# Kernel tuning notes

Measured on AMD Instinct MI355X. Metric: run time of the kernel, lower is better.

Reference implementation:

```python
import jax, jax.numpy as jnp
import numpy as np

VOCAB = 50000; T = 4096; EMBED = 500; H = 500  # hidden per direction (HIDDEN_SIZE=1000, bidirectional)
NUM_TAGS = 16; START = 14; STOP = 15
NEG = -10000.0


def setup_inputs() -> dict:
    key = jax.random.key(0)
    ks = jax.random.split(key, 16)
    n = lambda k, s, sc=0.1: (jax.random.normal(k, s) * sc).astype(jnp.float32)
    trans = n(ks[12], (NUM_TAGS, NUM_TAGS), 1.0)
    trans = trans.at[START, :].set(NEG).at[:, STOP].set(NEG)  # as in __init__
    return {
        "sent": jax.random.randint(ks[0], (T,), 0, VOCAB),
        "embed_w": n(ks[1], (VOCAB, EMBED), 1.0),
        "wih0": n(ks[2], (2, 4 * H, EMBED)),
        "whh0": n(ks[3], (2, 4 * H, H)),
        "bih0": n(ks[4], (2, 4 * H)),
        "bhh0": n(ks[5], (2, 4 * H)),
        "wih1": n(ks[6], (2, 4 * H, 2 * H)),
        "whh1": n(ks[7], (2, 4 * H, H)),
        "bih1": n(ks[8], (2, 4 * H)),
        "bhh1": n(ks[9], (2, 4 * H)),
        "w_out": n(ks[10], (NUM_TAGS, 2 * H)),
        "b_out": n(ks[11], (NUM_TAGS,)),
        "trans": trans,
        "h0": n(ks[13], (4, H), 1.0),  # init_hidden() uses randn; layout [layer*2+dir, H]
        "c0": n(ks[14], (4, H), 1.0),
    }


def _lstm_dir(x, wih, whh, bih, bhh, h0, c0):
    b = bih + bhh
    def cell(carry, xt):
        h, c = carry
        g = xt @ wih.T + h @ whh.T + b          # [4H], torch gate order i,f,g,o
        i, f, gg, o = jnp.split(g, 4)
        c = jax.nn.sigmoid(f) * c + jax.nn.sigmoid(i) * jnp.tanh(gg)
        h = jax.nn.sigmoid(o) * jnp.tanh(c)
        return (h, c), h
    _, hs = jax.lax.scan(cell, (h0, c0), x)
    return hs  # [T, H]


def _bilstm_layer(x, wih, whh, bih, bhh, h0, c0):
    fwd = _lstm_dir(x, wih[0], whh[0], bih[0], bhh[0], h0[0], c0[0])
    bwd = _lstm_dir(x[::-1], wih[1], whh[1], bih[1], bhh[1], h0[1], c0[1])[::-1]
    return jnp.concatenate([fwd, bwd], axis=-1)  # [T, 2H]


def _features(sent, embed_w, wih0, whh0, bih0, bhh0, wih1, whh1, bih1, bhh1, w_out, b_out, h0, c0):
    x = embed_w[sent]                                            # [T, EMBED]
    x = _bilstm_layer(x, wih0, whh0, bih0, bhh0, h0[0:2], c0[0:2])
    x = _bilstm_layer(x, wih1, whh1, bih1, bhh1, h0[2:4], c0[2:4])
    return x @ w_out.T + b_out                                   # [T, NUM_TAGS]


def _viterbi(feats, trans):
    score0 = jnp.full((NUM_TAGS,), NEG, dtype=feats.dtype).at[START].set(0.0)
    def step(score, feat):
        m = score[None, :] + trans               # m[tag, prev] = score[prev] + trans[tag, prev]
        return jnp.max(m, axis=1) + feat, jnp.argmax(m, axis=1)
    score, bptr = jax.lax.scan(step, score0, feats)              # bptr: [T, NUM_TAGS]
    score = score + trans[STOP]
    best_tag = jnp.argmax(score)
    best_score = score[best_tag]
    # faithful to the source backtrace: best_tag is NOT updated inside its loop,
    # so path = [bptr[1][bt], ..., bptr[T-1][bt], bt]
    path = jnp.concatenate([bptr[1:, best_tag], best_tag[None]])
    return best_score, path


def reference(sent, embed_w, wih0, whh0, bih0, bhh0, wih1, whh1, bih1, bhh1, w_out, b_out, trans, h0, c0):
    feats = _features(sent, embed_w, wih0, whh0, bih0, bhh0,
                      wih1, whh1, bih1, bhh1, w_out, b_out, h0, c0)
    return _viterbi(feats, trans)
```

## Files before the change

kernel.cpp:

```cpp
#include <hip/hip_runtime.h>


#define T_SEQ 4096
#define HPAD  512
#define NTAG  16


__global__ void zero_k(float* __restrict__ p, int n) {
  int i = blockIdx.x * blockDim.x + threadIdx.x;
  int stride = gridDim.x * blockDim.x;
  for (; i < n; i += stride) p[i] = 0.0f;
}

__global__ void embed_k(const int* __restrict__ sent, const float* __restrict__ ew,
                        float* __restrict__ x0) {
  int t = blockIdx.x;
  int row = sent[t];
  for (int k = threadIdx.x; k < HPAD; k += blockDim.x)
    x0[(size_t)t * HPAD + k] = (k < 500) ? ew[(size_t)row * 500 + k] : 0.0f;
}

__global__ __launch_bounds__(256) void gin_gemm_k(
    const float* __restrict__ A, int KA,
    const float* __restrict__ wih, const float* __restrict__ bih,
    const float* __restrict__ bhh, int Kreal, float* __restrict__ G) {
  const int dir = blockIdx.z;
  const int bm = blockIdx.y, bn = blockIdx.x;
  const float* W = wih + (size_t)dir * 2000 * Kreal;

  __shared__ float As[16][128];
  __shared__ float Bs[16][128];

  const int tid = threadIdx.x;
  const int tx = tid & 15, ty = tid >> 4;
  float acc[8][8] = {};

  for (int k0 = 0; k0 < KA; k0 += 16) {
#pragma unroll
    for (int q = 0; q < 2; q++) {
      int f4 = tid + q * 256;
      int m = f4 >> 2, kc = (f4 & 3) * 4;
      float4 av = *reinterpret_cast<const float4*>(A + (size_t)(bm * 128 + m) * KA + k0 + kc);
      As[kc + 0][m] = av.x; As[kc + 1][m] = av.y;
      As[kc + 2][m] = av.z; As[kc + 3][m] = av.w;
    }
#pragma unroll
    for (int q = 0; q < 2; q++) {
      int f4 = tid + q * 256;
      int n = f4 >> 2, kc = (f4 & 3) * 4;
      int nn = bn * 128 + n;
      int gate = nn >> 9, j = nn & 511;
#pragma unroll
      for (int e = 0; e < 4; e++) {
        int k = k0 + kc + e;
        int jk = k & 511, half = k >> 9;
        float v = 0.0f;
        if (j < 500 && jk < 500)
          v = W[(size_t)(gate * 500 + j) * Kreal + half * 500 + jk];
        Bs[kc + e][n] = v;
      }
    }
    __syncthreads();
#pragma unroll
    for (int kk = 0; kk < 16; kk++) {
      float a[8], b[8];
      *reinterpret_cast<float4*>(&a[0]) = *reinterpret_cast<const float4*>(&As[kk][ty * 8]);
      *reinterpret_cast<float4*>(&a[4]) = *reinterpret_cast<const float4*>(&As[kk][ty * 8 + 4]);
      *reinterpret_cast<float4*>(&b[0]) = *reinterpret_cast<const float4*>(&Bs[kk][tx * 8]);
      *reinterpret_cast<float4*>(&b[4]) = *reinterpret_cast<const float4*>(&Bs[kk][tx * 8 + 4]);
#pragma unroll
      for (int i = 0; i < 8; i++)
#pragma unroll
        for (int j = 0; j < 8; j++) acc[i][j] = fmaf(a[i], b[j], acc[i][j]);
    }
    __syncthreads();
  }
#pragma unroll
  for (int i = 0; i < 8; i++) {
#pragma unroll
    for (int j = 0; j < 8; j++) {
      int m = bm * 128 + ty * 8 + i;
      int nn = bn * 128 + tx * 8 + j;
      int gate = nn >> 9, ju = nn & 511;
      float o = 0.0f;
      if (ju < 500) {
        int r = gate * 500 + ju;
        o = acc[i][j] + bih[dir * 2000 + r] + bhh[dir * 2000 + r];
      }
      G[((size_t)dir * T_SEQ + m) * 2048 + nn] = o;
    }
  }
}

__device__ __forceinline__ unsigned long long pack_hv(unsigned tag, float h) {
  return (unsigned long long)tag | ((unsigned long long)__float_as_uint(h) << 32);
}

__device__ __forceinline__ float fsig(float x) {
  float e = __expf(-x);
  return __builtin_amdgcn_rcpf(1.0f + e);
}
__device__ __forceinline__ float ftanhf(float x) {
  return fmaf(2.0f, fsig(x + x), -1.0f);
}

__global__ void hinit_k(const float* __restrict__ h0, int layer,
                        unsigned long long* __restrict__ hcomm) {
  int i = blockIdx.x * blockDim.x + threadIdx.x;
  int dir = i >> 10, par = (i >> 9) & 1, j = i & 511;
  unsigned long long v;
  if (par == 0) {
    float h = (j < 500) ? h0[(layer * 2 + dir) * 500 + j] : 0.0f;
    v = pack_hv(0u, h);
  } else {
    v = 0xFFFFFFFFull;
  }
  hcomm[(size_t)(dir * 2 + par) * HPAD + j] = v;
}

__global__ __launch_bounds__(1024)
__attribute__((amdgpu_waves_per_eu(4, 4)))
void lstm_k(
    const float* __restrict__ whh_base,
    const float* __restrict__ gin,
    const float* __restrict__ c0,
    float* __restrict__ xout,
    unsigned long long* __restrict__ hcomm,
    int layer) {
  __shared__ float part[16][68];
  __shared__ float hbuf[16][32];

  const int tid = threadIdx.x;
  const int dir = blockIdx.x >> 5;
  const int wgd = blockIdx.x & 31;
  const int w = tid >> 6;
  const int lane = tid & 63;

  const int gate = lane >> 4;
  const int ul   = lane & 15;
  const int j    = wgd * 16 + ul;
  const int row  = gate * 500 + j;

  float wreg[32];
  const float* Wd = whh_base + (size_t)dir * 2000 * 500;
#pragma unroll
  for (int i = 0; i < 32; i++) {
    int k = w * 32 + i;
    wreg[i] = (j < 500 && k < 500) ? Wd[(size_t)row * 500 + k] : 0.0f;
  }
#pragma unroll
  for (int i = 0; i < 32; i++) asm volatile("" : "+v"(wreg[i]));

  float c = 0.0f;
  if (w == 0 && lane < 16 && j < 500) c = c0[(layer * 2 + dir) * 500 + j];

  unsigned long long* hcd = hcomm + (size_t)dir * 2 * HPAD;
  bool dead = false;

  for (int t = 0; t < T_SEQ; t++) {
    const int t_in = (dir == 0) ? t : (T_SEQ - 1 - t);

    float gi = 0.0f;
    if (w == 0) {
      const float* gb = gin + ((size_t)dir * T_SEQ + t_in) * 2048;
      gi = gb[gate * 512 + j];
    }

    unsigned long long v = 0;
    if (!dead) {
      const unsigned long long* hp =
          hcd + (size_t)(t & 1) * HPAD + w * 32 + (lane & 31);
      int guard = 0;
      for (;;) {
        v = __hip_atomic_load(hp, __ATOMIC_RELAXED, __HIP_MEMORY_SCOPE_AGENT);
        if (__all((int)((unsigned)v == (unsigned)t))) break;
        if (++guard > (1 << 22)) { dead = true; break; }
      }
    }
    float hval = __uint_as_float((unsigned)(v >> 32));

    if (lane < 32) hbuf[w][lane] = hval;
    float a = 0.0f;
#pragma unroll
    for (int b = 0; b < 8; b++) {
      float4 hv = *reinterpret_cast<const float4*>(&hbuf[w][b * 4]);
      a = fmaf(wreg[b * 4 + 0], hv.x, a);
      a = fmaf(wreg[b * 4 + 1], hv.y, a);
      a = fmaf(wreg[b * 4 + 2], hv.z, a);
      a = fmaf(wreg[b * 4 + 3], hv.w, a);
    }
    part[w][lane] = a;
    __syncthreads();

    if (w == 0) {
      __builtin_amdgcn_s_setprio(1);
      float s = gi;
#pragma unroll
      for (int q = 0; q < 16; q++) s += part[q][lane];
      float nl = (gate == 2) ? ftanhf(s) : fsig(s);
      float xf = __shfl(nl, lane + 16, 64);
      float xg = __shfl(nl, lane + 32, 64);
      float xo = __shfl(nl, lane + 48, 64);
      if (lane < 16) {
        c = xf * c + nl * xg;
        float h = xo * ftanhf(c);
        __hip_atomic_store(hcd + (size_t)((t + 1) & 1) * HPAD + j,
                           pack_hv((unsigned)(t + 1), h),
                           __ATOMIC_RELAXED, __HIP_MEMORY_SCOPE_AGENT);
        if (j < 500)
          xout[(size_t)t_in * 1024 + (size_t)dir * HPAD + j] = h;
      }
      __builtin_amdgcn_s_setprio(0);
    }
  }
}

__global__ __launch_bounds__(256) void feats_k(
    const float* __restrict__ x2, const float* __restrict__ w_out,
    const float* __restrict__ b_out, float* __restrict__ feats) {
  int tid = threadIdx.x;
  int tag = tid & 15, tl = tid >> 4;
  int t = blockIdx.x * 16 + tl;
  float acc = 0.0f;
  for (int k = 0; k < 1024; k++) {
    int jk = k & 511;
    if (jk < 500)
      acc = fmaf(x2[(size_t)t * 1024 + k], w_out[tag * 1000 + (k >> 9) * 500 + jk], acc);
  }
  feats[t * 16 + tag] = acc + b_out[tag];
}

__global__ __launch_bounds__(256) void viterbi_k(
    const float* __restrict__ feats, const float* __restrict__ trans,
    int* __restrict__ bptr, float* __restrict__ out) {
  __shared__ float sfin[NTAG];
  __shared__ int sbest;
  int tid = threadIdx.x;
  if (tid < 64) {
    int tag = tid & 15;
    float treg[16];
#pragma unroll
    for (int p = 0; p < 16; p++) treg[p] = trans[tag * 16 + p];
    float s = (tag == 14) ? 0.0f : -10000.0f;
    for (int t = 0; t < T_SEQ; t++) {
      float best = -3.4e38f;
      int barg = 0;
#pragma unroll
      for (int p = 0; p < 16; p++) {
        float cand = __shfl(s, p, 16) + treg[p];
        if (cand > best) { best = cand; barg = p; }
      }
      s = best + feats[t * 16 + tag];
      if (tid < 16) bptr[t * 16 + tag] = barg;
    }
    s += trans[15 * 16 + tag];
    if (tid < 16) sfin[tag] = s;
  }
  __syncthreads();
  if (tid == 0) {
    float best = -3.4e38f;
    int bt = 0;
    for (int p = 0; p < 16; p++) {
      float vv = sfin[p];
      if (vv > best) { best = vv; bt = p; }
    }
    out[0] = best;
    sbest = bt;
  }
  __syncthreads();
  int bt = sbest;
  for (int i = tid; i < T_SEQ - 1; i += blockDim.x)
    out[1 + i] = (float)bptr[(i + 1) * 16 + bt];
  if (tid == 0) out[T_SEQ] = (float)bt;
}

extern "C" void kernel_launch(void* const* d_in, const int* in_sizes, int n_in,
                              void* d_out, int out_size, void* d_ws, size_t ws_size,
                              hipStream_t stream) {
  const int*   sent  = (const int*)d_in[0];
  const float* embed = (const float*)d_in[1];
  const float* wih0  = (const float*)d_in[2];
  const float* whh0  = (const float*)d_in[3];
  const float* bih0  = (const float*)d_in[4];
  const float* bhh0  = (const float*)d_in[5];
  const float* wih1  = (const float*)d_in[6];
  const float* whh1  = (const float*)d_in[7];
  const float* bih1  = (const float*)d_in[8];
  const float* bhh1  = (const float*)d_in[9];
  const float* w_out = (const float*)d_in[10];
  const float* b_out = (const float*)d_in[11];
  const float* trans = (const float*)d_in[12];
  const float* h0    = (const float*)d_in[13];
  const float* c0    = (const float*)d_in[14];
  float* out = (float*)d_out;

  char* ws = (char*)d_ws;
  float* x0    = (float*)(ws + 0);
  float* x1    = (float*)(ws + 8388608);
  float* x2    = (float*)(ws + 25165824);
  float* gin   = (float*)(ws + 41943040);
  float* feats = (float*)(ws + 109051904);
  int*   bptr  = (int*)(ws + 109314048);
  unsigned long long* hcomm = (unsigned long long*)(ws + 109576192);

  zero_k<<<2048, 256, 0, stream>>>(x1, 2 * T_SEQ * 1024);
  embed_k<<<T_SEQ, 256, 0, stream>>>(sent, embed, x0);

  gin_gemm_k<<<dim3(16, 32, 2), 256, 0, stream>>>(x0, 512, wih0, bih0, bhh0, 500, gin);
  hinit_k<<<2, 1024, 0, stream>>>(h0, 0, hcomm);
  lstm_k<<<64, 1024, 0, stream>>>(whh0, gin, c0, x1, hcomm, 0);

  gin_gemm_k<<<dim3(16, 32, 2), 256, 0, stream>>>(x1, 1024, wih1, bih1, bhh1, 1000, gin);
  hinit_k<<<2, 1024, 0, stream>>>(h0, 1, hcomm);
  lstm_k<<<64, 1024, 0, stream>>>(whh1, gin, c0, x2, hcomm, 1);

  feats_k<<<T_SEQ / 16, 256, 0, stream>>>(x2, w_out, b_out, feats);
  viterbi_k<<<1, 256, 0, stream>>>(feats, trans, bptr, out);
}
```

Measured before the change: 13.76 ms.

## Vectorize weight loads, prefetch spin loads, tree-reduce partials, parallelize Viterbi max

Several independent tweaks land together. The GEMM B-tile load becomes a float4 load, and the LSTM spin-wait keeps three atomic loads in flight. The 16 partial sums are tree-reduced to shorten the serial add chain, feats_k uses four accumulators, and Viterbi splits the 16-way max across 4 lane groups with xor shuffles and prefetches feats. The x1 zeroing kernel is dropped; this assumes padding columns never need zeroing. It also relies on float4 alignment of W rows (Kreal 500/1000, so 16-byte aligned) and changes the argmax tie-break order.

```diff
diff --git a/kernel.cpp b/kernel.cpp
--- a/kernel.cpp
+++ b/kernel.cpp
@@ -5,12 +5,6 @@
 #define HPAD  512
 #define NTAG  16
 
-
-__global__ void zero_k(float* __restrict__ p, int n) {
-  int i = blockIdx.x * blockDim.x + threadIdx.x;
-  int stride = gridDim.x * blockDim.x;
-  for (; i < n; i += stride) p[i] = 0.0f;
-}
 
 __global__ void embed_k(const int* __restrict__ sent, const float* __restrict__ ew,
                         float* __restrict__ x0) {
@@ -50,15 +44,14 @@
       int n = f4 >> 2, kc = (f4 & 3) * 4;
       int nn = bn * 128 + n;
       int gate = nn >> 9, j = nn & 511;
-#pragma unroll
-      for (int e = 0; e < 4; e++) {
-        int k = k0 + kc + e;
-        int jk = k & 511, half = k >> 9;
-        float v = 0.0f;
-        if (j < 500 && jk < 500)
-          v = W[(size_t)(gate * 500 + j) * Kreal + half * 500 + jk];
-        Bs[kc + e][n] = v;
-      }
+      int k = k0 + kc;
+      int jk = k & 511, half = k >> 9;
+      float4 bv = {0.0f, 0.0f, 0.0f, 0.0f};
+      if (j < 500 && jk < 500)
+        bv = *reinterpret_cast<const float4*>(
+            &W[(size_t)(gate * 500 + j) * Kreal + half * 500 + jk]);
+      Bs[kc + 0][n] = bv.x; Bs[kc + 1][n] = bv.y;
+      Bs[kc + 2][n] = bv.z; Bs[kc + 3][n] = bv.w;
     }
     __syncthreads();
 #pragma unroll
@@ -170,10 +163,14 @@
     if (!dead) {
       const unsigned long long* hp =
           hcd + (size_t)(t & 1) * HPAD + w * 32 + (lane & 31);
+      unsigned long long va = __hip_atomic_load(hp, __ATOMIC_RELAXED, __HIP_MEMORY_SCOPE_AGENT);
+      unsigned long long vb = __hip_atomic_load(hp, __ATOMIC_RELAXED, __HIP_MEMORY_SCOPE_AGENT);
+      unsigned long long vc = __hip_atomic_load(hp, __ATOMIC_RELAXED, __HIP_MEMORY_SCOPE_AGENT);
       int guard = 0;
       for (;;) {
-        v = __hip_atomic_load(hp, __ATOMIC_RELAXED, __HIP_MEMORY_SCOPE_AGENT);
-        if (__all((int)((unsigned)v == (unsigned)t))) break;
+        if (__all((int)((unsigned)va == (unsigned)t))) { v = va; break; }
+        va = vb; vb = vc;
+        vc = __hip_atomic_load(hp, __ATOMIC_RELAXED, __HIP_MEMORY_SCOPE_AGENT);
         if (++guard > (1 << 22)) { dead = true; break; }
       }
     }
@@ -194,9 +191,16 @@
 
     if (w == 0) {
       __builtin_amdgcn_s_setprio(1);
-      float s = gi;
-#pragma unroll
-      for (int q = 0; q < 16; q++) s += part[q][lane];
+      float p0 = part[0][lane] + part[1][lane];
+      float p1 = part[2][lane] + part[3][lane];
+      float p2 = part[4][lane] + part[5][lane];
+      float p3 = part[6][lane] + part[7][lane];
+      float p4 = part[8][lane] + part[9][lane];
+      float p5 = part[10][lane] + part[11][lane];
+      float p6 = part[12][lane] + part[13][lane];
+      float p7 = part[14][lane] + part[15][lane];
+      float q0 = p0 + p1, q1 = p2 + p3, q2 = p4 + p5, q3 = p6 + p7;
+      float s = gi + ((q0 + q1) + (q2 + q3));
       float nl = (gate == 2) ? ftanhf(s) : fsig(s);
       float xf = __shfl(nl, lane + 16, 64);
       float xg = __shfl(nl, lane + 32, 64);
@@ -221,55 +225,63 @@
   int tid = threadIdx.x;
   int tag = tid & 15, tl = tid >> 4;
   int t = blockIdx.x * 16 + tl;
-  float acc = 0.0f;
-  for (int k = 0; k < 1024; k++) {
+  float a0 = 0.0f, a1 = 0.0f, a2 = 0.0f, a3 = 0.0f;
+  for (int k = 0; k < 1024; k += 4) {
     int jk = k & 511;
-    if (jk < 500)
-      acc = fmaf(x2[(size_t)t * 1024 + k], w_out[tag * 1000 + (k >> 9) * 500 + jk], acc);
-  }
-  feats[t * 16 + tag] = acc + b_out[tag];
-}
-
-__global__ __launch_bounds__(256) void viterbi_k(
+    const float* xr = x2 + (size_t)t * 1024 + k;
+    const float* wr = w_out + tag * 1000 + (k >> 9) * 500 + jk;
+    if (jk + 3 < 500) {
+      a0 = fmaf(xr[0], wr[0], a0);
+      a1 = fmaf(xr[1], wr[1], a1);
+      a2 = fmaf(xr[2], wr[2], a2);
+      a3 = fmaf(xr[3], wr[3], a3);
+    } else if (jk < 500) {
+#pragma unroll
+      for (int e = 0; e < 4; e++)
+        if (jk + e < 500) a0 = fmaf(xr[e], wr[e], a0);
+    }
+  }
+  feats[t * 16 + tag] = ((a0 + a1) + (a2 + a3)) + b_out[tag];
+}
+
+__global__ __launch_bounds__(64) void viterbi_k(
     const float* __restrict__ feats, const float* __restrict__ trans,
     int* __restrict__ bptr, float* __restrict__ out) {
-  __shared__ float sfin[NTAG];
-  __shared__ int sbest;
   int tid = threadIdx.x;
-  if (tid < 64) {
-    int tag = tid & 15;
-    float treg[16];
-#pragma unroll
-    for (int p = 0; p < 16; p++) treg[p] = trans[tag * 16 + p];
-    float s = (tag == 14) ? 0.0f : -10000.0f;
-    for (int t = 0; t < T_SEQ; t++) {
-      float best = -3.4e38f;
-      int barg = 0;
-#pragma unroll
-      for (int p = 0; p < 16; p++) {
-        float cand = __shfl(s, p, 16) + treg[p];
-        if (cand > best) { best = cand; barg = p; }
-      }
-      s = best + feats[t * 16 + tag];
-      if (tid < 16) bptr[t * 16 + tag] = barg;
-    }
-    s += trans[15 * 16 + tag];
-    if (tid < 16) sfin[tag] = s;
-  }
-  __syncthreads();
-  if (tid == 0) {
-    float best = -3.4e38f;
-    int bt = 0;
-    for (int p = 0; p < 16; p++) {
-      float vv = sfin[p];
-      if (vv > best) { best = vv; bt = p; }
-    }
-    out[0] = best;
-    sbest = bt;
-  }
-  __syncthreads();
-  int bt = sbest;
-  for (int i = tid; i < T_SEQ - 1; i += blockDim.x)
+  int tag = tid & 15, pg = tid >> 4;
+  float tr0 = trans[tag * 16 + pg * 4 + 0];
+  float tr1 = trans[tag * 16 + pg * 4 + 1];
+  float tr2 = trans[tag * 16 + pg * 4 + 2];
+  float tr3 = trans[tag * 16 + pg * 4 + 3];
+  float s = (tag == 14) ? 0.0f : -10000.0f;
+  float ft = feats[tag];
+  for (int t = 0; t < T_SEQ; t++) {
+    float ftn = (t + 1 < T_SEQ) ? feats[(t + 1) * 16 + tag] : 0.0f;
+    float c0 = __shfl(s, pg * 4 + 0, 64) + tr0;
+    float c1 = __shfl(s, pg * 4 + 1, 64) + tr1;
+    float c2 = __shfl(s, pg * 4 + 2, 64) + tr2;
+    float c3 = __shfl(s, pg * 4 + 3, 64) + tr3;
+    float bv = c0; int bi = pg * 4;
+    if (c1 > bv) { bv = c1; bi = pg * 4 + 1; }
+    if (c2 > bv) { bv = c2; bi = pg * 4 + 2; }
+    if (c3 > bv) { bv = c3; bi = pg * 4 + 3; }
+    float ov = __shfl_xor(bv, 16, 64); int oi = __shfl_xor(bi, 16, 64);
+    if (ov > bv || (ov == bv && oi < bi)) { bv = ov; bi = oi; }
+    ov = __shfl_xor(bv, 32, 64); oi = __shfl_xor(bi, 32, 64);
+    if (ov > bv || (ov == bv && oi < bi)) { bv = ov; bi = oi; }
+    s = bv + ft;
+    ft = ftn;
+    if (pg == 0) bptr[t * 16 + tag] = bi;
+  }
+  s += trans[15 * 16 + tag];
+  float bv = s; int bi = tag;
+  for (int mask = 1; mask < 16; mask <<= 1) {
+    float ov = __shfl_xor(bv, mask, 16); int oi = __shfl_xor(bi, mask, 16);
+    if (ov > bv || (ov == bv && oi < bi)) { bv = ov; bi = oi; }
+  }
+  if (tid == 0) out[0] = bv;
+  int bt = bi;
+  for (int i = tid; i < T_SEQ - 1; i += 64)
     out[1 + i] = (float)bptr[(i + 1) * 16 + bt];
   if (tid == 0) out[T_SEQ] = (float)bt;
 }
@@ -303,7 +315,6 @@
   int*   bptr  = (int*)(ws + 109314048);
   unsigned long long* hcomm = (unsigned long long*)(ws + 109576192);
 
-  zero_k<<<2048, 256, 0, stream>>>(x1, 2 * T_SEQ * 1024);
   embed_k<<<T_SEQ, 256, 0, stream>>>(sent, embed, x0);
 
   gin_gemm_k<<<dim3(16, 32, 2), 256, 0, stream>>>(x0, 512, wih0, bih0, bhh0, 500, gin);
@@ -315,5 +326,5 @@
   lstm_k<<<64, 1024, 0, stream>>>(whh1, gin, c0, x2, hcomm, 1);
 
   feats_k<<<T_SEQ / 16, 256, 0, stream>>>(x2, w_out, b_out, feats);
-  viterbi_k<<<1, 256, 0, stream>>>(feats, trans, bptr, out);
-}
+  viterbi_k<<<1, 64, 0, stream>>>(feats, trans, bptr, out);
+}
```

After: 15.48 ms. 12.5% more time.
